# Optimization experiments

Measured on AMD Instinct MI355X. Metric: run time of the kernel, lower is better.

Reference implementation:

```python
import jax, jax.numpy as jnp
import numpy as np

M, K, N = 4096, 4096, 11008

def setup_inputs() -> dict:
    key = jax.random.key(0)
    k1, k2, k3, k4 = jax.random.split(key, 4)
    x = jax.random.normal(k1, (M, K), dtype=jnp.float32)
    weight = jax.random.randint(k2, (K, N), 0, 127, dtype=jnp.int32)
    antiquant_scale = jax.random.uniform(k3, (N,), dtype=jnp.float32)
    antiquant_offset = jax.random.normal(k4, (N,), dtype=jnp.float32)
    return {"x": x, "weight": weight, "antiquant_scale": antiquant_scale, "antiquant_offset": antiquant_offset}

def reference(x, weight, antiquant_scale, antiquant_offset):
    # Dequantize: (w + offset) * scale, per output channel (broadcast over K)
    dequantized_weight = (weight.astype(jnp.float32) + antiquant_offset) * antiquant_scale  # [K, N]
    return jnp.matmul(x, dequantized_weight)  # [M, N]
```

## Files before the change

### kernel.cpp

```cpp
#include <hip/hip_runtime.h>
#include <hip/hip_bf16.h>
#include <stdint.h>

#define M_DIM 4096
#define K_DIM 4096
#define N_DIM 11008
#define BKT 64
#define NT (K_DIM / BKT)
#define GRID_MN 688
#define NBLK_M 16

typedef __attribute__((ext_vector_type(8))) short short8;
typedef __attribute__((ext_vector_type(4))) float floatx4;

__device__ __forceinline__ short f2bf(float f) {
  union { float f; uint32_t u; } c; c.f = f;
  uint32_t u = c.u;
  u += 0x7FFFu + ((u >> 16) & 1u);
  return (short)(u >> 16);
}

__device__ __forceinline__ void gload_lds16(const void* g, void* l) {
  __builtin_amdgcn_global_load_lds(
      (const __attribute__((address_space(1))) unsigned int*)g,
      (__attribute__((address_space(3))) unsigned int*)l, 16, 0, 0);
}

__global__ __launch_bounds__(256) void convert_x_kernel(const float* __restrict__ x,
                                                        short* __restrict__ xb,
                                                        float* __restrict__ rowsum) {
  const int m = blockIdx.x;
  const int t = threadIdx.x;
  const float* row = x + (size_t)m * K_DIM + t * 16;
  short* orow = xb + (size_t)m * K_DIM + t * 16;
  float4 v0 = *(const float4*)(row + 0);
  float4 v1 = *(const float4*)(row + 4);
  float4 v2 = *(const float4*)(row + 8);
  float4 v3 = *(const float4*)(row + 12);
  float sum = v0.x + v0.y + v0.z + v0.w
            + v1.x + v1.y + v1.z + v1.w
            + v2.x + v2.y + v2.z + v2.w
            + v3.x + v3.y + v3.z + v3.w;
  short8 o0, o1;
  o0[0] = f2bf(v0.x); o0[1] = f2bf(v0.y); o0[2] = f2bf(v0.z); o0[3] = f2bf(v0.w);
  o0[4] = f2bf(v1.x); o0[5] = f2bf(v1.y); o0[6] = f2bf(v1.z); o0[7] = f2bf(v1.w);
  o1[0] = f2bf(v2.x); o1[1] = f2bf(v2.y); o1[2] = f2bf(v2.z); o1[3] = f2bf(v2.w);
  o1[4] = f2bf(v3.x); o1[5] = f2bf(v3.y); o1[6] = f2bf(v3.z); o1[7] = f2bf(v3.w);
  *(short8*)(orow) = o0;
  *(short8*)(orow + 8) = o1;
  #pragma unroll
  for (int off = 32; off > 0; off >>= 1) sum += __shfl_down(sum, off);
  __shared__ float part[4];
  if ((t & 63) == 0) part[t >> 6] = sum;
  __syncthreads();
  if (t == 0) rowsum[m] = part[0] + part[1] + part[2] + part[3];
}

__global__ __launch_bounds__(256) void convert_w_kernel(const int* __restrict__ w,
                                                        short* __restrict__ wt) {
  __shared__ short tile[64][72];
  const int bk = blockIdx.x * 64;
  const int bn = blockIdx.y * 64;
  const int t = threadIdx.x;
  const int kr = t >> 2;
  const int c0 = (t & 3) * 16;
  const int* src = w + (size_t)(bk + kr) * N_DIM + bn + c0;
  int4 a = *(const int4*)(src + 0);
  int4 b = *(const int4*)(src + 4);
  int4 c = *(const int4*)(src + 8);
  int4 d = *(const int4*)(src + 12);
  short* dst = &tile[kr][c0];
  dst[0]  = f2bf((float)a.x); dst[1]  = f2bf((float)a.y);
  dst[2]  = f2bf((float)a.z); dst[3]  = f2bf((float)a.w);
  dst[4]  = f2bf((float)b.x); dst[5]  = f2bf((float)b.y);
  dst[6]  = f2bf((float)b.z); dst[7]  = f2bf((float)b.w);
  dst[8]  = f2bf((float)c.x); dst[9]  = f2bf((float)c.y);
  dst[10] = f2bf((float)c.z); dst[11] = f2bf((float)c.w);
  dst[12] = f2bf((float)d.x); dst[13] = f2bf((float)d.y);
  dst[14] = f2bf((float)d.z); dst[15] = f2bf((float)d.w);
  __syncthreads();
  const int nr = t >> 2;
  short8 o0, o1;
  #pragma unroll
  for (int j = 0; j < 8; ++j) o0[j] = tile[c0 + j][nr];
  #pragma unroll
  for (int j = 0; j < 8; ++j) o1[j] = tile[c0 + 8 + j][nr];
  short* odst = wt + (size_t)(bn + nr) * K_DIM + bk + c0;
  *(short8*)(odst) = o0;
  *(short8*)(odst + 8) = o1;
}

__global__ __launch_bounds__(512, 2) void gemm_kernel(const short* __restrict__ xb,
                                                      const short* __restrict__ wt,
                                                      const float* __restrict__ scale,
                                                      const float* __restrict__ offset,
                                                      const float* __restrict__ rowsum,
                                                      float* __restrict__ out) {
  __shared__ short lds[2][4][8192];
  const int tid = threadIdx.x;
  const int bid = blockIdx.x;
  const int wg = (bid & 7) * (GRID_MN / 8) + (bid >> 3);
  const int bm = (wg % NBLK_M) * 256;
  const int bn = (wg / NBLK_M) * 256;

  const int wid = tid >> 6;
  const int lane = tid & 63;
  const int wr = wid >> 2;
  const int wc = wid & 3;
  const int hb = wc >> 1;
  const int lr = lane & 15;
  const int lg = lane >> 4;
  const int swz = lr & 7;
  const int gk0 = (lg ^ swz) * 8;
  const int gk1 = ((lg ^ 4) ^ swz) * 8;
  const int brow = (wc & 1) * 64 + lr;

  const int srow = tid >> 3;
  const int glog = (tid & 7) ^ (srow & 7);

  auto stage = [&](const short* opbase, int rowbase, int half, int kt, short* region) {
    const short* s0 = opbase + (size_t)(rowbase + half * 128 + srow) * K_DIM + kt * BKT + glog * 8;
    gload_lds16(s0, (char*)region + tid * 16);
    const short* s1 = opbase + (size_t)(rowbase + half * 128 + srow + 64) * K_DIM + kt * BKT + glog * 8;
    gload_lds16(s1, (char*)region + (tid + 512) * 16);
  };

  floatx4 acc[8][4];
  const floatx4 zero = {0.f, 0.f, 0.f, 0.f};
  #pragma unroll
  for (int i = 0; i < 8; ++i)
    #pragma unroll
    for (int j = 0; j < 4; ++j) acc[i][j] = zero;

  stage(xb, bm, 0, 0, &lds[0][0][0]);
  stage(xb, bm, 1, 0, &lds[0][1][0]);
  stage(wt, bn, 0, 0, &lds[0][2][0]);
  stage(wt, bn, 1, 0, &lds[0][3][0]);
  stage(wt, bn, 0, 1, &lds[1][2][0]);
  stage(xb, bm, 0, 1, &lds[1][0][0]);
  stage(wt, bn, 1, 1, &lds[1][3][0]);
  asm volatile("s_waitcnt vmcnt(6)" ::: "memory");
  __builtin_amdgcn_s_barrier();

  short8 a03[4][2], a47[4][2], b0[2][2], b1[2][2];
  {
    const short* As = &lds[0][wr][0];
    #pragma unroll
    for (int mf = 0; mf < 4; ++mf) {
      const short* p = As + (mf * 16 + lr) * 64;
      a03[mf][0] = *(const short8*)(p + gk0);
      a03[mf][1] = *(const short8*)(p + gk1);
    }
  }

  for (int s = 0; s < NT; ++s) {
    const int beta = s & 1;
    const short* As = &lds[beta][wr][0];
    const short* Bs = &lds[beta][2 + hb][0];

    #pragma unroll
    for (int nf = 0; nf < 2; ++nf) {
      const short* p = Bs + (brow + nf * 16) * 64;
      b0[nf][0] = *(const short8*)(p + gk0);
      b0[nf][1] = *(const short8*)(p + gk1);
      const short* q = Bs + (brow + (nf + 2) * 16) * 64;
      b1[nf][0] = *(const short8*)(q + gk0);
      b1[nf][1] = *(const short8*)(q + gk1);
    }
    asm volatile("s_waitcnt lgkmcnt(8)" ::: "memory");
    if (s + 1 < NT) stage(xb, bm, 1, s + 1, &lds[beta ^ 1][1][0]);
    __builtin_amdgcn_s_barrier();
    asm volatile("s_waitcnt lgkmcnt(0)" ::: "memory");
    __builtin_amdgcn_s_setprio(1);
    #pragma unroll
    for (int mf = 0; mf < 4; ++mf)
      #pragma unroll
      for (int nf = 0; nf < 2; ++nf) {
        acc[mf][nf] = __builtin_amdgcn_mfma_f32_16x16x32_bf16(a03[mf][0], b0[nf][0], acc[mf][nf], 0, 0, 0);
        acc[mf][nf] = __builtin_amdgcn_mfma_f32_16x16x32_bf16(a03[mf][1], b0[nf][1], acc[mf][nf], 0, 0, 0);
      }
    __builtin_amdgcn_s_setprio(0);
    __builtin_amdgcn_s_barrier();

    #pragma unroll
    for (int mf = 0; mf < 4; ++mf) {
      const short* p = As + ((mf + 4) * 16 + lr) * 64;
      a47[mf][0] = *(const short8*)(p + gk0);
      a47[mf][1] = *(const short8*)(p + gk1);
    }
    if (s + 2 < NT) stage(wt, bn, 0, s + 2, &lds[beta][2][0]);
    __builtin_amdgcn_s_barrier();
    asm volatile("s_waitcnt lgkmcnt(0)" ::: "memory");
    __builtin_amdgcn_s_setprio(1);
    #pragma unroll
    for (int mf = 0; mf < 4; ++mf)
      #pragma unroll
      for (int nf = 0; nf < 2; ++nf) {
        acc[mf + 4][nf] = __builtin_amdgcn_mfma_f32_16x16x32_bf16(a47[mf][0], b0[nf][0], acc[mf + 4][nf], 0, 0, 0);
        acc[mf + 4][nf] = __builtin_amdgcn_mfma_f32_16x16x32_bf16(a47[mf][1], b0[nf][1], acc[mf + 4][nf], 0, 0, 0);
      }
    __builtin_amdgcn_s_setprio(0);
    __builtin_amdgcn_s_barrier();

    if (s + 2 < NT) stage(xb, bm, 0, s + 2, &lds[beta][0][0]);
    __builtin_amdgcn_s_barrier();
    __builtin_amdgcn_s_setprio(1);
    #pragma unroll
    for (int mf = 0; mf < 4; ++mf)
      #pragma unroll
      for (int nf = 0; nf < 2; ++nf) {
        acc[mf][nf + 2] = __builtin_amdgcn_mfma_f32_16x16x32_bf16(a03[mf][0], b1[nf][0], acc[mf][nf + 2], 0, 0, 0);
        acc[mf][nf + 2] = __builtin_amdgcn_mfma_f32_16x16x32_bf16(a03[mf][1], b1[nf][1], acc[mf][nf + 2], 0, 0, 0);
      }
    __builtin_amdgcn_s_setprio(0);
    __builtin_amdgcn_s_barrier();

    if (s + 2 < NT) {
      stage(wt, bn, 1, s + 2, &lds[beta][3][0]);
      asm volatile("s_waitcnt vmcnt(6)" ::: "memory");
    } else {
      asm volatile("s_waitcnt vmcnt(0)" ::: "memory");
    }
    __builtin_amdgcn_s_barrier();
    if (s + 1 < NT) {
      const short* An = &lds[beta ^ 1][wr][0];
      #pragma unroll
      for (int mf = 0; mf < 4; ++mf) {
        const short* p = An + (mf * 16 + lr) * 64;
        a03[mf][0] = *(const short8*)(p + gk0);
        a03[mf][1] = *(const short8*)(p + gk1);
      }
    }
    __builtin_amdgcn_s_setprio(1);
    #pragma unroll
    for (int mf = 0; mf < 4; ++mf)
      #pragma unroll
      for (int nf = 0; nf < 2; ++nf) {
        acc[mf + 4][nf + 2] = __builtin_amdgcn_mfma_f32_16x16x32_bf16(a47[mf][0], b1[nf][0], acc[mf + 4][nf + 2], 0, 0, 0);
        acc[mf + 4][nf + 2] = __builtin_amdgcn_mfma_f32_16x16x32_bf16(a47[mf][1], b1[nf][1], acc[mf + 4][nf + 2], 0, 0, 0);
      }
    __builtin_amdgcn_s_setprio(0);
    __builtin_amdgcn_s_barrier();
  }

  const int orow0 = bm + wr * 128 + lg * 4;
  const int ocol0 = bn + wc * 64 + lr;
  float4 rsv[8];
  #pragma unroll
  for (int amf = 0; amf < 8; ++amf)
    rsv[amf] = *(const float4*)&rowsum[orow0 + amf * 16];
  #pragma unroll
  for (int anf = 0; anf < 4; ++anf) {
    const int n = ocol0 + anf * 16;
    const float sc = scale[n];
    const float of = offset[n];
    #pragma unroll
    for (int amf = 0; amf < 8; ++amf) {
      const int mbase = orow0 + amf * 16;
      const float4 rv = rsv[amf];
      out[(size_t)(mbase + 0) * N_DIM + n] = (acc[amf][anf][0] + of * rv.x) * sc;
      out[(size_t)(mbase + 1) * N_DIM + n] = (acc[amf][anf][1] + of * rv.y) * sc;
      out[(size_t)(mbase + 2) * N_DIM + n] = (acc[amf][anf][2] + of * rv.z) * sc;
      out[(size_t)(mbase + 3) * N_DIM + n] = (acc[amf][anf][3] + of * rv.w) * sc;
    }
  }
}

__global__ __launch_bounds__(256) void fallback_gemm(const float* __restrict__ x,
                                                     const int* __restrict__ w,
                                                     const float* __restrict__ scale,
                                                     const float* __restrict__ offset,
                                                     float* __restrict__ out) {
  __shared__ float xs[32][33];
  __shared__ float bs[32][33];
  const int bm = blockIdx.y * 32, bn = blockIdx.x * 32;
  const int t = threadIdx.x;
  const int tm = t >> 5, tn = t & 31;
  float acc[4] = {0.f, 0.f, 0.f, 0.f};
  for (int k0 = 0; k0 < K_DIM; k0 += 32) {
    #pragma unroll
    for (int i = 0; i < 4; ++i) {
      int idx = t + i * 256; int r = idx >> 5, c = idx & 31;
      xs[r][c] = x[(size_t)(bm + r) * K_DIM + k0 + c];
      bs[r][c] = ((float)w[(size_t)(k0 + r) * N_DIM + bn + c] + offset[bn + c]) * scale[bn + c];
    }
    __syncthreads();
    #pragma unroll 8
    for (int kk = 0; kk < 32; ++kk) {
      float wv = bs[kk][tn];
      #pragma unroll
      for (int i = 0; i < 4; ++i) acc[i] += xs[tm + 8 * i][kk] * wv;
    }
    __syncthreads();
  }
  #pragma unroll
  for (int i = 0; i < 4; ++i)
    out[(size_t)(bm + tm + 8 * i) * N_DIM + bn + tn] = acc[i];
}

extern "C" void kernel_launch(void* const* d_in, const int* in_sizes, int n_in,
                              void* d_out, int out_size, void* d_ws, size_t ws_size,
                              hipStream_t stream) {
  const float* x      = (const float*)d_in[0];
  const int*   w      = (const int*)d_in[1];
  const float* scale  = (const float*)d_in[2];
  const float* offset = (const float*)d_in[3];
  float* out = (float*)d_out;

  const size_t xb_bytes = (size_t)M_DIM * K_DIM * 2;
  const size_t wt_bytes = (size_t)N_DIM * K_DIM * 2;
  const size_t rs_bytes = (size_t)M_DIM * 4;

  if (ws_size >= xb_bytes + wt_bytes + rs_bytes) {
    short* xb = (short*)d_ws;
    short* wt = (short*)((char*)d_ws + xb_bytes);
    float* rowsum = (float*)((char*)d_ws + xb_bytes + wt_bytes);
    convert_x_kernel<<<M_DIM, 256, 0, stream>>>(x, xb, rowsum);
    convert_w_kernel<<<dim3(K_DIM / 64, N_DIM / 64), 256, 0, stream>>>(w, wt);
    gemm_kernel<<<GRID_MN, 512, 0, stream>>>(xb, wt, scale, offset, rowsum, out);
  } else {
    fallback_gemm<<<dim3(N_DIM / 32, M_DIM / 32), 256, 0, stream>>>(x, w, scale, offset, out);
  }
}
```

Measured before the change: 423.6 us.

## Restructure main loop schedule to overlap LDS fragment loads with MFMA phases

Reorders the software pipeline of the bf16 MFMA main loop. b0 fragments for the next tile are now loaded alongside a03 at the end of each iteration, and b1 and a47 reads are interleaved between MFMA quadrants with partial lgkmcnt waits. Global-to-LDS staging is redistributed across the phases, and the prologue prefetch order changes to wait for the first tile fully. The intent is fewer barriers per iteration (five instead of eight) and LDS reads hidden behind MFMA work. The risk is more live registers and subtle LDS race hazards from the new wait counts.

```diff
diff --git a/kernel.cpp b/kernel.cpp
--- a/kernel.cpp
+++ b/kernel.cpp
@@ -136,10 +136,7 @@
   stage(xb, bm, 1, 0, &lds[0][1][0]);
   stage(wt, bn, 0, 0, &lds[0][2][0]);
   stage(wt, bn, 1, 0, &lds[0][3][0]);
-  stage(wt, bn, 0, 1, &lds[1][2][0]);
-  stage(xb, bm, 0, 1, &lds[1][0][0]);
-  stage(wt, bn, 1, 1, &lds[1][3][0]);
-  asm volatile("s_waitcnt vmcnt(6)" ::: "memory");
+  asm volatile("s_waitcnt vmcnt(0)" ::: "memory");
   __builtin_amdgcn_s_barrier();
 
   short8 a03[4][2], a47[4][2], b0[2][2], b1[2][2];
@@ -151,36 +148,22 @@
       a03[mf][0] = *(const short8*)(p + gk0);
       a03[mf][1] = *(const short8*)(p + gk1);
     }
-  }
-
-  for (int s = 0; s < NT; ++s) {
-    const int beta = s & 1;
-    const short* As = &lds[beta][wr][0];
-    const short* Bs = &lds[beta][2 + hb][0];
-
+    const short* Bsp = &lds[0][2 + hb][0];
     #pragma unroll
     for (int nf = 0; nf < 2; ++nf) {
-      const short* p = Bs + (brow + nf * 16) * 64;
+      const short* p = Bsp + (brow + nf * 16) * 64;
       b0[nf][0] = *(const short8*)(p + gk0);
       b0[nf][1] = *(const short8*)(p + gk1);
-      const short* q = Bs + (brow + (nf + 2) * 16) * 64;
-      b1[nf][0] = *(const short8*)(q + gk0);
-      b1[nf][1] = *(const short8*)(q + gk1);
-    }
-    asm volatile("s_waitcnt lgkmcnt(8)" ::: "memory");
-    if (s + 1 < NT) stage(xb, bm, 1, s + 1, &lds[beta ^ 1][1][0]);
-    __builtin_amdgcn_s_barrier();
-    asm volatile("s_waitcnt lgkmcnt(0)" ::: "memory");
-    __builtin_amdgcn_s_setprio(1);
-    #pragma unroll
-    for (int mf = 0; mf < 4; ++mf)
-      #pragma unroll
-      for (int nf = 0; nf < 2; ++nf) {
-        acc[mf][nf] = __builtin_amdgcn_mfma_f32_16x16x32_bf16(a03[mf][0], b0[nf][0], acc[mf][nf], 0, 0, 0);
-        acc[mf][nf] = __builtin_amdgcn_mfma_f32_16x16x32_bf16(a03[mf][1], b0[nf][1], acc[mf][nf], 0, 0, 0);
-      }
-    __builtin_amdgcn_s_setprio(0);
-    __builtin_amdgcn_s_barrier();
+    }
+  }
+  stage(xb, bm, 0, 1, &lds[1][0][0]);
+  stage(wt, bn, 0, 1, &lds[1][2][0]);
+  stage(wt, bn, 1, 1, &lds[1][3][0]);
+
+  for (int u = 0; u < NT; ++u) {
+    const int g = u & 1;
+    const short* As = &lds[g][wr][0];
+    const short* Bs = &lds[g][2 + hb][0];
 
     #pragma unroll
     for (int mf = 0; mf < 4; ++mf) {
@@ -188,9 +171,28 @@
       a47[mf][0] = *(const short8*)(p + gk0);
       a47[mf][1] = *(const short8*)(p + gk1);
     }
-    if (s + 2 < NT) stage(wt, bn, 0, s + 2, &lds[beta][2][0]);
+    asm volatile("s_waitcnt lgkmcnt(8)" ::: "memory");
     __builtin_amdgcn_s_barrier();
-    asm volatile("s_waitcnt lgkmcnt(0)" ::: "memory");
+    if (u + 1 < NT) stage(xb, bm, 1, u + 1, &lds[g ^ 1][1][0]);
+    __builtin_amdgcn_s_setprio(1);
+    #pragma unroll
+    for (int mf = 0; mf < 4; ++mf)
+      #pragma unroll
+      for (int nf = 0; nf < 2; ++nf) {
+        acc[mf][nf] = __builtin_amdgcn_mfma_f32_16x16x32_bf16(a03[mf][0], b0[nf][0], acc[mf][nf], 0, 0, 0);
+        acc[mf][nf] = __builtin_amdgcn_mfma_f32_16x16x32_bf16(a03[mf][1], b0[nf][1], acc[mf][nf], 0, 0, 0);
+      }
+    __builtin_amdgcn_s_setprio(0);
+
+    #pragma unroll
+    for (int nf = 0; nf < 2; ++nf) {
+      const short* q = Bs + (brow + (nf + 2) * 16) * 64;
+      b1[nf][0] = *(const short8*)(q + gk0);
+      b1[nf][1] = *(const short8*)(q + gk1);
+    }
+    asm volatile("s_waitcnt lgkmcnt(4)" ::: "memory");
+    __builtin_amdgcn_s_barrier();
+    if (u + 2 < NT) stage(xb, bm, 0, u + 2, &lds[g][0][0]);
     __builtin_amdgcn_s_setprio(1);
     #pragma unroll
     for (int mf = 0; mf < 4; ++mf)
@@ -200,10 +202,10 @@
         acc[mf + 4][nf] = __builtin_amdgcn_mfma_f32_16x16x32_bf16(a47[mf][1], b0[nf][1], acc[mf + 4][nf], 0, 0, 0);
       }
     __builtin_amdgcn_s_setprio(0);
+
+    asm volatile("s_waitcnt lgkmcnt(0)" ::: "memory");
     __builtin_amdgcn_s_barrier();
-
-    if (s + 2 < NT) stage(xb, bm, 0, s + 2, &lds[beta][0][0]);
-    __builtin_amdgcn_s_barrier();
+    if (u + 2 < NT) stage(wt, bn, 0, u + 2, &lds[g][2][0]);
     __builtin_amdgcn_s_setprio(1);
     #pragma unroll
     for (int mf = 0; mf < 4; ++mf)
@@ -213,23 +215,29 @@
         acc[mf][nf + 2] = __builtin_amdgcn_mfma_f32_16x16x32_bf16(a03[mf][1], b1[nf][1], acc[mf][nf + 2], 0, 0, 0);
       }
     __builtin_amdgcn_s_setprio(0);
-    __builtin_amdgcn_s_barrier();
-
-    if (s + 2 < NT) {
-      stage(wt, bn, 1, s + 2, &lds[beta][3][0]);
+
+    if (u + 2 < NT) {
+      stage(wt, bn, 1, u + 2, &lds[g][3][0]);
       asm volatile("s_waitcnt vmcnt(6)" ::: "memory");
     } else {
       asm volatile("s_waitcnt vmcnt(0)" ::: "memory");
     }
     __builtin_amdgcn_s_barrier();
-    if (s + 1 < NT) {
-      const short* An = &lds[beta ^ 1][wr][0];
+    if (u + 1 < NT) {
+      const short* An = &lds[g ^ 1][wr][0];
+      const short* Bn = &lds[g ^ 1][2 + hb][0];
       #pragma unroll
       for (int mf = 0; mf < 4; ++mf) {
         const short* p = An + (mf * 16 + lr) * 64;
         a03[mf][0] = *(const short8*)(p + gk0);
         a03[mf][1] = *(const short8*)(p + gk1);
       }
+      #pragma unroll
+      for (int nf = 0; nf < 2; ++nf) {
+        const short* p = Bn + (brow + nf * 16) * 64;
+        b0[nf][0] = *(const short8*)(p + gk0);
+        b0[nf][1] = *(const short8*)(p + gk1);
+      }
     }
     __builtin_amdgcn_s_setprio(1);
     #pragma unroll
@@ -240,7 +248,6 @@
         acc[mf + 4][nf + 2] = __builtin_amdgcn_mfma_f32_16x16x32_bf16(a47[mf][1], b1[nf][1], acc[mf + 4][nf + 2], 0, 0, 0);
       }
     __builtin_amdgcn_s_setprio(0);
-    __builtin_amdgcn_s_barrier();
   }
 
   const int orow0 = bm + wr * 128 + lg * 4;
```

Result: faster. 405.0 us, median of 2 (-4.4%).

## Restructure GEMM main loop: unroll by two, reschedule LDS reads and barriers

Applied to the files above, without the earlier changes.

Unrolls the K loop by two so the double-buffer index is a compile-time constant, and replaces per-call address recomputation with incrementing global pointers. It also moves the fragment loads: a47 and b1 are read earlier and the next tile's b0 is prefetched together with a03. The number of barriers per step drops from eight to four. The aim is to cut address arithmetic and synchronisation overhead and overlap LDS reads with MFMA, at the risk of LDS read/write hazards with the new wait counts.

```diff
diff --git a/kernel.cpp b/kernel.cpp
--- a/kernel.cpp
+++ b/kernel.cpp
@@ -118,11 +118,15 @@
   const int srow = tid >> 3;
   const int glog = (tid & 7) ^ (srow & 7);
 
-  auto stage = [&](const short* opbase, int rowbase, int half, int kt, short* region) {
-    const short* s0 = opbase + (size_t)(rowbase + half * 128 + srow) * K_DIM + kt * BKT + glog * 8;
-    gload_lds16(s0, (char*)region + tid * 16);
-    const short* s1 = opbase + (size_t)(rowbase + half * 128 + srow + 64) * K_DIM + kt * BKT + glog * 8;
-    gload_lds16(s1, (char*)region + (tid + 512) * 16);
+  const size_t toff = (size_t)srow * K_DIM + glog * 8;
+  const short* pA0 = xb + (size_t)bm * K_DIM + toff;
+  const short* pA1 = xb + ((size_t)bm + 128) * K_DIM + toff;
+  const short* pB0 = wt + (size_t)bn * K_DIM + toff;
+  const short* pB1 = wt + ((size_t)bn + 128) * K_DIM + toff;
+
+  auto stage2 = [&](const short* p, short* region) {
+    gload_lds16(p, (char*)region + tid * 16);
+    gload_lds16(p + (size_t)64 * K_DIM, (char*)region + (tid + 512) * 16);
   };
 
   floatx4 acc[8][4];
@@ -132,116 +136,142 @@
     #pragma unroll
     for (int j = 0; j < 4; ++j) acc[i][j] = zero;
 
-  stage(xb, bm, 0, 0, &lds[0][0][0]);
-  stage(xb, bm, 1, 0, &lds[0][1][0]);
-  stage(wt, bn, 0, 0, &lds[0][2][0]);
-  stage(wt, bn, 1, 0, &lds[0][3][0]);
-  stage(wt, bn, 0, 1, &lds[1][2][0]);
-  stage(xb, bm, 0, 1, &lds[1][0][0]);
-  stage(wt, bn, 1, 1, &lds[1][3][0]);
+  stage2(pA0, &lds[0][0][0]);
+  stage2(pA1, &lds[0][1][0]);
+  stage2(pB0, &lds[0][2][0]);
+  stage2(pB1, &lds[0][3][0]);
+  stage2(pB0 + BKT, &lds[1][2][0]);
+  stage2(pA0 + BKT, &lds[1][0][0]);
+  stage2(pB1 + BKT, &lds[1][3][0]);
   asm volatile("s_waitcnt vmcnt(6)" ::: "memory");
   __builtin_amdgcn_s_barrier();
+  pA1 += BKT;
+  pA0 += 2 * BKT;
+  pB0 += 2 * BKT;
+  pB1 += 2 * BKT;
+
+  const short* const AsB[2] = {&lds[0][wr][0], &lds[1][wr][0]};
+  const short* const BsB[2] = {&lds[0][2 + hb][0], &lds[1][2 + hb][0]};
 
   short8 a03[4][2], a47[4][2], b0[2][2], b1[2][2];
   {
-    const short* As = &lds[0][wr][0];
+    const short* As = AsB[0];
     #pragma unroll
     for (int mf = 0; mf < 4; ++mf) {
       const short* p = As + (mf * 16 + lr) * 64;
       a03[mf][0] = *(const short8*)(p + gk0);
       a03[mf][1] = *(const short8*)(p + gk1);
     }
-  }
-
-  for (int s = 0; s < NT; ++s) {
-    const int beta = s & 1;
-    const short* As = &lds[beta][wr][0];
-    const short* Bs = &lds[beta][2 + hb][0];
-
+    const short* Bsp = BsB[0];
     #pragma unroll
     for (int nf = 0; nf < 2; ++nf) {
-      const short* p = Bs + (brow + nf * 16) * 64;
+      const short* p = Bsp + (brow + nf * 16) * 64;
       b0[nf][0] = *(const short8*)(p + gk0);
       b0[nf][1] = *(const short8*)(p + gk1);
-      const short* q = Bs + (brow + (nf + 2) * 16) * 64;
-      b1[nf][0] = *(const short8*)(q + gk0);
-      b1[nf][1] = *(const short8*)(q + gk1);
-    }
-    asm volatile("s_waitcnt lgkmcnt(8)" ::: "memory");
-    if (s + 1 < NT) stage(xb, bm, 1, s + 1, &lds[beta ^ 1][1][0]);
-    __builtin_amdgcn_s_barrier();
-    asm volatile("s_waitcnt lgkmcnt(0)" ::: "memory");
-    __builtin_amdgcn_s_setprio(1);
-    #pragma unroll
-    for (int mf = 0; mf < 4; ++mf)
-      #pragma unroll
-      for (int nf = 0; nf < 2; ++nf) {
-        acc[mf][nf] = __builtin_amdgcn_mfma_f32_16x16x32_bf16(a03[mf][0], b0[nf][0], acc[mf][nf], 0, 0, 0);
-        acc[mf][nf] = __builtin_amdgcn_mfma_f32_16x16x32_bf16(a03[mf][1], b0[nf][1], acc[mf][nf], 0, 0, 0);
-      }
-    __builtin_amdgcn_s_setprio(0);
-    __builtin_amdgcn_s_barrier();
-
-    #pragma unroll
-    for (int mf = 0; mf < 4; ++mf) {
-      const short* p = As + ((mf + 4) * 16 + lr) * 64;
-      a47[mf][0] = *(const short8*)(p + gk0);
-      a47[mf][1] = *(const short8*)(p + gk1);
-    }
-    if (s + 2 < NT) stage(wt, bn, 0, s + 2, &lds[beta][2][0]);
-    __builtin_amdgcn_s_barrier();
-    asm volatile("s_waitcnt lgkmcnt(0)" ::: "memory");
-    __builtin_amdgcn_s_setprio(1);
-    #pragma unroll
-    for (int mf = 0; mf < 4; ++mf)
-      #pragma unroll
-      for (int nf = 0; nf < 2; ++nf) {
-        acc[mf + 4][nf] = __builtin_amdgcn_mfma_f32_16x16x32_bf16(a47[mf][0], b0[nf][0], acc[mf + 4][nf], 0, 0, 0);
-        acc[mf + 4][nf] = __builtin_amdgcn_mfma_f32_16x16x32_bf16(a47[mf][1], b0[nf][1], acc[mf + 4][nf], 0, 0, 0);
-      }
-    __builtin_amdgcn_s_setprio(0);
-    __builtin_amdgcn_s_barrier();
-
-    if (s + 2 < NT) stage(xb, bm, 0, s + 2, &lds[beta][0][0]);
-    __builtin_amdgcn_s_barrier();
-    __builtin_amdgcn_s_setprio(1);
-    #pragma unroll
-    for (int mf = 0; mf < 4; ++mf)
-      #pragma unroll
-      for (int nf = 0; nf < 2; ++nf) {
-        acc[mf][nf + 2] = __builtin_amdgcn_mfma_f32_16x16x32_bf16(a03[mf][0], b1[nf][0], acc[mf][nf + 2], 0, 0, 0);
-        acc[mf][nf + 2] = __builtin_amdgcn_mfma_f32_16x16x32_bf16(a03[mf][1], b1[nf][1], acc[mf][nf + 2], 0, 0, 0);
-      }
-    __builtin_amdgcn_s_setprio(0);
-    __builtin_amdgcn_s_barrier();
-
-    if (s + 2 < NT) {
-      stage(wt, bn, 1, s + 2, &lds[beta][3][0]);
-      asm volatile("s_waitcnt vmcnt(6)" ::: "memory");
-    } else {
-      asm volatile("s_waitcnt vmcnt(0)" ::: "memory");
-    }
-    __builtin_amdgcn_s_barrier();
-    if (s + 1 < NT) {
-      const short* An = &lds[beta ^ 1][wr][0];
-      #pragma unroll
-      for (int mf = 0; mf < 4; ++mf) {
-        const short* p = An + (mf * 16 + lr) * 64;
-        a03[mf][0] = *(const short8*)(p + gk0);
-        a03[mf][1] = *(const short8*)(p + gk1);
-      }
-    }
-    __builtin_amdgcn_s_setprio(1);
-    #pragma unroll
-    for (int mf = 0; mf < 4; ++mf)
-      #pragma unroll
-      for (int nf = 0; nf < 2; ++nf) {
-        acc[mf + 4][nf + 2] = __builtin_amdgcn_mfma_f32_16x16x32_bf16(a47[mf][0], b1[nf][0], acc[mf + 4][nf + 2], 0, 0, 0);
-        acc[mf + 4][nf + 2] = __builtin_amdgcn_mfma_f32_16x16x32_bf16(a47[mf][1], b1[nf][1], acc[mf + 4][nf + 2], 0, 0, 0);
-      }
-    __builtin_amdgcn_s_setprio(0);
-    __builtin_amdgcn_s_barrier();
-  }
+    }
+  }
+
+#define STEP_BODY(G, GN)                                                       \
+  {                                                                            \
+    const short* As = AsB[G];                                                  \
+    const short* Bs = BsB[G];                                                  \
+                    \
+    _Pragma("unroll")                                                          \
+    for (int mf = 0; mf < 4; ++mf) {                                           \
+      const short* p = As + ((mf + 4) * 16 + lr) * 64;                         \
+      a47[mf][0] = *(const short8*)(p + gk0);                                  \
+      a47[mf][1] = *(const short8*)(p + gk1);                                  \
+    }                                                                          \
+    asm volatile("s_waitcnt lgkmcnt(8)" ::: "memory");                         \
+    __builtin_amdgcn_s_barrier();                                              \
+    if (u + 1 < NT) stage2(pA1, &lds[GN][1][0]);                               \
+    pA1 += BKT;                                                                \
+    __builtin_amdgcn_s_setprio(1);                                             \
+    _Pragma("unroll")                                                          \
+    for (int mf = 0; mf < 4; ++mf)                                             \
+      _Pragma("unroll")                                                        \
+      for (int nf = 0; nf < 2; ++nf) {                                         \
+        acc[mf][nf] = __builtin_amdgcn_mfma_f32_16x16x32_bf16(a03[mf][0], b0[nf][0], acc[mf][nf], 0, 0, 0); \
+        acc[mf][nf] = __builtin_amdgcn_mfma_f32_16x16x32_bf16(a03[mf][1], b0[nf][1], acc[mf][nf], 0, 0, 0); \
+      }                                                                        \
+    __builtin_amdgcn_s_setprio(0);                                             \
+                      \
+    _Pragma("unroll")                                                          \
+    for (int nf = 0; nf < 2; ++nf) {                                           \
+      const short* q = Bs + (brow + (nf + 2) * 16) * 64;                       \
+      b1[nf][0] = *(const short8*)(q + gk0);                                   \
+      b1[nf][1] = *(const short8*)(q + gk1);                                   \
+    }                                                                          \
+    asm volatile("s_waitcnt lgkmcnt(4)" ::: "memory");                         \
+    __builtin_amdgcn_s_barrier();                                              \
+    if (u + 2 < NT) stage2(pA0, &lds[G][0][0]);                                \
+    pA0 += BKT;                                                                \
+    __builtin_amdgcn_s_setprio(1);                                             \
+    _Pragma("unroll")                                                          \
+    for (int mf = 0; mf < 4; ++mf)                                             \
+      _Pragma("unroll")                                                        \
+      for (int nf = 0; nf < 2; ++nf) {                                         \
+        acc[mf + 4][nf] = __builtin_amdgcn_mfma_f32_16x16x32_bf16(a47[mf][0], b0[nf][0], acc[mf + 4][nf], 0, 0, 0); \
+        acc[mf + 4][nf] = __builtin_amdgcn_mfma_f32_16x16x32_bf16(a47[mf][1], b0[nf][1], acc[mf + 4][nf], 0, 0, 0); \
+      }                                                                        \
+    __builtin_amdgcn_s_setprio(0);                                             \
+                                  \
+    asm volatile("s_waitcnt lgkmcnt(0)" ::: "memory");                         \
+    __builtin_amdgcn_s_barrier();                                              \
+    if (u + 2 < NT) stage2(pB0, &lds[G][2][0]);                                \
+    pB0 += BKT;                                                                \
+    __builtin_amdgcn_s_setprio(1);                                             \
+    _Pragma("unroll")                                                          \
+    for (int mf = 0; mf < 4; ++mf)                                             \
+      _Pragma("unroll")                                                        \
+      for (int nf = 0; nf < 2; ++nf) {                                         \
+        acc[mf][nf + 2] = __builtin_amdgcn_mfma_f32_16x16x32_bf16(a03[mf][0], b1[nf][0], acc[mf][nf + 2], 0, 0, 0); \
+        acc[mf][nf + 2] = __builtin_amdgcn_mfma_f32_16x16x32_bf16(a03[mf][1], b1[nf][1], acc[mf][nf + 2], 0, 0, 0); \
+      }                                                                        \
+    __builtin_amdgcn_s_setprio(0);                                             \
+      \
+    if (u + 2 < NT) {                                                          \
+      stage2(pB1, &lds[G][3][0]);                                              \
+      asm volatile("s_waitcnt vmcnt(6)" ::: "memory");                         \
+    } else {                                                                   \
+      asm volatile("s_waitcnt vmcnt(0)" ::: "memory");                         \
+    }                                                                          \
+    pB1 += BKT;                                                                \
+    __builtin_amdgcn_s_barrier();                                              \
+    if (u + 1 < NT) {                                                          \
+      const short* An = AsB[GN];                                               \
+      const short* Bn = BsB[GN];                                               \
+      _Pragma("unroll")                                                        \
+      for (int mf = 0; mf < 4; ++mf) {                                         \
+        const short* p = An + (mf * 16 + lr) * 64;                             \
+        a03[mf][0] = *(const short8*)(p + gk0);                                \
+        a03[mf][1] = *(const short8*)(p + gk1);                                \
+      }                                                                        \
+      _Pragma("unroll")                                                        \
+      for (int nf = 0; nf < 2; ++nf) {                                         \
+        const short* p = Bn + (brow + nf * 16) * 64;                           \
+        b0[nf][0] = *(const short8*)(p + gk0);                                 \
+        b0[nf][1] = *(const short8*)(p + gk1);                                 \
+      }                                                                        \
+    }                                                                          \
+    __builtin_amdgcn_s_setprio(1);                                             \
+    _Pragma("unroll")                                                          \
+    for (int mf = 0; mf < 4; ++mf)                                             \
+      _Pragma("unroll")                                                        \
+      for (int nf = 0; nf < 2; ++nf) {                                         \
+        acc[mf + 4][nf + 2] = __builtin_amdgcn_mfma_f32_16x16x32_bf16(a47[mf][0], b1[nf][0], acc[mf + 4][nf + 2], 0, 0, 0); \
+        acc[mf + 4][nf + 2] = __builtin_amdgcn_mfma_f32_16x16x32_bf16(a47[mf][1], b1[nf][1], acc[mf + 4][nf + 2], 0, 0, 0); \
+      }                                                                        \
+    __builtin_amdgcn_s_setprio(0);                                             \
+  }
+
+  for (int u = 0; u < NT; u += 2) {
+    STEP_BODY(0, 1)
+    ++u;
+    STEP_BODY(1, 0)
+    --u;
+  }
+#undef STEP_BODY
 
   const int orow0 = bm + wr * 128 + lg * 4;
   const int ocol0 = bn + wc * 64 + lr;
```

Result: faster. 405.6 us (-4.2%).

## Unroll K-loop by two with incremental pointers and reordered LDS staging schedule

Applied to the files above, without the earlier changes.

Restructures the main GEMM loop into a two-stage unrolled form with compile-time buffer indices. Global-to-LDS source pointers are precomputed and advanced incrementally, which removes per-stage address arithmetic. The staging order and the B-fragment reads are changed, with B1 now read just before its quadrant, and the vmcnt waits are adjusted. Sched barriers after the lgkm waits are added and the tail is peeled. This aims to cut scalar/VALU overhead and improve overlap, but it adds code size and needs the wait counts to match the new issue order.

```diff
diff --git a/kernel.cpp b/kernel.cpp
--- a/kernel.cpp
+++ b/kernel.cpp
@@ -12,6 +12,13 @@
 
 typedef __attribute__((ext_vector_type(8))) short short8;
 typedef __attribute__((ext_vector_type(4))) float floatx4;
+
+#define MFMA16 __builtin_amdgcn_mfma_f32_16x16x32_bf16
+#define BAR() __builtin_amdgcn_s_barrier()
+#define LGKM0() do { asm volatile("s_waitcnt lgkmcnt(0)" ::: "memory"); __builtin_amdgcn_sched_barrier(0); } while (0)
+#define LGKM8() asm volatile("s_waitcnt lgkmcnt(8)" ::: "memory")
+#define VM4() asm volatile("s_waitcnt vmcnt(4)" ::: "memory")
+#define VM0() asm volatile("s_waitcnt vmcnt(0)" ::: "memory")
 
 __device__ __forceinline__ short f2bf(float f) {
   union { float f; uint32_t u; } c; c.f = f;
@@ -117,12 +124,15 @@
 
   const int srow = tid >> 3;
   const int glog = (tid & 7) ^ (srow & 7);
-
-  auto stage = [&](const short* opbase, int rowbase, int half, int kt, short* region) {
-    const short* s0 = opbase + (size_t)(rowbase + half * 128 + srow) * K_DIM + kt * BKT + glog * 8;
-    gload_lds16(s0, (char*)region + tid * 16);
-    const short* s1 = opbase + (size_t)(rowbase + half * 128 + srow + 64) * K_DIM + kt * BKT + glog * 8;
-    gload_lds16(s1, (char*)region + (tid + 512) * 16);
+  const size_t toff = (size_t)srow * K_DIM + glog * 8;
+  const short* pAh0 = xb + (size_t)bm * K_DIM + toff;
+  const short* pAh1 = xb + ((size_t)bm + 128) * K_DIM + toff;
+  const short* pBh0 = wt + (size_t)bn * K_DIM + toff;
+  const short* pBh1 = wt + ((size_t)bn + 128) * K_DIM + toff;
+
+  auto stage2 = [&](const short* p, short* region) {
+    gload_lds16(p, (char*)region + tid * 16);
+    gload_lds16(p + (size_t)64 * K_DIM, (char*)region + (tid + 512) * 16);
   };
 
   floatx4 acc[8][4];
@@ -132,116 +142,144 @@
     #pragma unroll
     for (int j = 0; j < 4; ++j) acc[i][j] = zero;
 
-  stage(xb, bm, 0, 0, &lds[0][0][0]);
-  stage(xb, bm, 1, 0, &lds[0][1][0]);
-  stage(wt, bn, 0, 0, &lds[0][2][0]);
-  stage(wt, bn, 1, 0, &lds[0][3][0]);
-  stage(wt, bn, 0, 1, &lds[1][2][0]);
-  stage(xb, bm, 0, 1, &lds[1][0][0]);
-  stage(wt, bn, 1, 1, &lds[1][3][0]);
-  asm volatile("s_waitcnt vmcnt(6)" ::: "memory");
-  __builtin_amdgcn_s_barrier();
-
   short8 a03[4][2], a47[4][2], b0[2][2], b1[2][2];
-  {
-    const short* As = &lds[0][wr][0];
+  const short* const As[2] = {&lds[0][wr][0], &lds[1][wr][0]};
+  const short* const Bs[2] = {&lds[0][2 + hb][0], &lds[1][2 + hb][0]};
+
+  auto rdA03 = [&](const short* A) {
     #pragma unroll
     for (int mf = 0; mf < 4; ++mf) {
-      const short* p = As + (mf * 16 + lr) * 64;
+      const short* p = A + (mf * 16 + lr) * 64;
       a03[mf][0] = *(const short8*)(p + gk0);
       a03[mf][1] = *(const short8*)(p + gk1);
     }
-  }
-
-  for (int s = 0; s < NT; ++s) {
-    const int beta = s & 1;
-    const short* As = &lds[beta][wr][0];
-    const short* Bs = &lds[beta][2 + hb][0];
-
+  };
+  auto rdA47 = [&](const short* A) {
+    #pragma unroll
+    for (int mf = 0; mf < 4; ++mf) {
+      const short* p = A + ((mf + 4) * 16 + lr) * 64;
+      a47[mf][0] = *(const short8*)(p + gk0);
+      a47[mf][1] = *(const short8*)(p + gk1);
+    }
+  };
+  auto rdB0 = [&](const short* B) {
     #pragma unroll
     for (int nf = 0; nf < 2; ++nf) {
-      const short* p = Bs + (brow + nf * 16) * 64;
+      const short* p = B + (brow + nf * 16) * 64;
       b0[nf][0] = *(const short8*)(p + gk0);
       b0[nf][1] = *(const short8*)(p + gk1);
-      const short* q = Bs + (brow + (nf + 2) * 16) * 64;
-      b1[nf][0] = *(const short8*)(q + gk0);
-      b1[nf][1] = *(const short8*)(q + gk1);
-    }
-    asm volatile("s_waitcnt lgkmcnt(8)" ::: "memory");
-    if (s + 1 < NT) stage(xb, bm, 1, s + 1, &lds[beta ^ 1][1][0]);
-    __builtin_amdgcn_s_barrier();
-    asm volatile("s_waitcnt lgkmcnt(0)" ::: "memory");
+    }
+  };
+  auto rdB1 = [&](const short* B) {
+    #pragma unroll
+    for (int nf = 0; nf < 2; ++nf) {
+      const short* p = B + (brow + (nf + 2) * 16) * 64;
+      b1[nf][0] = *(const short8*)(p + gk0);
+      b1[nf][1] = *(const short8*)(p + gk1);
+    }
+  };
+  auto q00 = [&]() {
     __builtin_amdgcn_s_setprio(1);
     #pragma unroll
     for (int mf = 0; mf < 4; ++mf)
       #pragma unroll
       for (int nf = 0; nf < 2; ++nf) {
-        acc[mf][nf] = __builtin_amdgcn_mfma_f32_16x16x32_bf16(a03[mf][0], b0[nf][0], acc[mf][nf], 0, 0, 0);
-        acc[mf][nf] = __builtin_amdgcn_mfma_f32_16x16x32_bf16(a03[mf][1], b0[nf][1], acc[mf][nf], 0, 0, 0);
+        acc[mf][nf] = MFMA16(a03[mf][0], b0[nf][0], acc[mf][nf], 0, 0, 0);
+        acc[mf][nf] = MFMA16(a03[mf][1], b0[nf][1], acc[mf][nf], 0, 0, 0);
       }
     __builtin_amdgcn_s_setprio(0);
-    __builtin_amdgcn_s_barrier();
-
-    #pragma unroll
-    for (int mf = 0; mf < 4; ++mf) {
-      const short* p = As + ((mf + 4) * 16 + lr) * 64;
-      a47[mf][0] = *(const short8*)(p + gk0);
-      a47[mf][1] = *(const short8*)(p + gk1);
-    }
-    if (s + 2 < NT) stage(wt, bn, 0, s + 2, &lds[beta][2][0]);
-    __builtin_amdgcn_s_barrier();
-    asm volatile("s_waitcnt lgkmcnt(0)" ::: "memory");
+  };
+  auto q10 = [&]() {
     __builtin_amdgcn_s_setprio(1);
     #pragma unroll
     for (int mf = 0; mf < 4; ++mf)
       #pragma unroll
       for (int nf = 0; nf < 2; ++nf) {
-        acc[mf + 4][nf] = __builtin_amdgcn_mfma_f32_16x16x32_bf16(a47[mf][0], b0[nf][0], acc[mf + 4][nf], 0, 0, 0);
-        acc[mf + 4][nf] = __builtin_amdgcn_mfma_f32_16x16x32_bf16(a47[mf][1], b0[nf][1], acc[mf + 4][nf], 0, 0, 0);
+        acc[mf + 4][nf] = MFMA16(a47[mf][0], b0[nf][0], acc[mf + 4][nf], 0, 0, 0);
+        acc[mf + 4][nf] = MFMA16(a47[mf][1], b0[nf][1], acc[mf + 4][nf], 0, 0, 0);
       }
     __builtin_amdgcn_s_setprio(0);
-    __builtin_amdgcn_s_barrier();
-
-    if (s + 2 < NT) stage(xb, bm, 0, s + 2, &lds[beta][0][0]);
-    __builtin_amdgcn_s_barrier();
+  };
+  auto q01 = [&]() {
     __builtin_amdgcn_s_setprio(1);
     #pragma unroll
     for (int mf = 0; mf < 4; ++mf)
       #pragma unroll
       for (int nf = 0; nf < 2; ++nf) {
-        acc[mf][nf + 2] = __builtin_amdgcn_mfma_f32_16x16x32_bf16(a03[mf][0], b1[nf][0], acc[mf][nf + 2], 0, 0, 0);
-        acc[mf][nf + 2] = __builtin_amdgcn_mfma_f32_16x16x32_bf16(a03[mf][1], b1[nf][1], acc[mf][nf + 2], 0, 0, 0);
+        acc[mf][nf + 2] = MFMA16(a03[mf][0], b1[nf][0], acc[mf][nf + 2], 0, 0, 0);
+        acc[mf][nf + 2] = MFMA16(a03[mf][1], b1[nf][1], acc[mf][nf + 2], 0, 0, 0);
       }
     __builtin_amdgcn_s_setprio(0);
-    __builtin_amdgcn_s_barrier();
-
-    if (s + 2 < NT) {
-      stage(wt, bn, 1, s + 2, &lds[beta][3][0]);
-      asm volatile("s_waitcnt vmcnt(6)" ::: "memory");
-    } else {
-      asm volatile("s_waitcnt vmcnt(0)" ::: "memory");
-    }
-    __builtin_amdgcn_s_barrier();
-    if (s + 1 < NT) {
-      const short* An = &lds[beta ^ 1][wr][0];
-      #pragma unroll
-      for (int mf = 0; mf < 4; ++mf) {
-        const short* p = An + (mf * 16 + lr) * 64;
-        a03[mf][0] = *(const short8*)(p + gk0);
-        a03[mf][1] = *(const short8*)(p + gk1);
-      }
-    }
+  };
+  auto q11 = [&]() {
     __builtin_amdgcn_s_setprio(1);
     #pragma unroll
     for (int mf = 0; mf < 4; ++mf)
       #pragma unroll
       for (int nf = 0; nf < 2; ++nf) {
-        acc[mf + 4][nf + 2] = __builtin_amdgcn_mfma_f32_16x16x32_bf16(a47[mf][0], b1[nf][0], acc[mf + 4][nf + 2], 0, 0, 0);
-        acc[mf + 4][nf + 2] = __builtin_amdgcn_mfma_f32_16x16x32_bf16(a47[mf][1], b1[nf][1], acc[mf + 4][nf + 2], 0, 0, 0);
+        acc[mf + 4][nf + 2] = MFMA16(a47[mf][0], b1[nf][0], acc[mf + 4][nf + 2], 0, 0, 0);
+        acc[mf + 4][nf + 2] = MFMA16(a47[mf][1], b1[nf][1], acc[mf + 4][nf + 2], 0, 0, 0);
       }
     __builtin_amdgcn_s_setprio(0);
-    __builtin_amdgcn_s_barrier();
+  };
+
+  stage2(pAh0, &lds[0][0][0]); pAh0 += BKT;
+  stage2(pBh0, &lds[0][2][0]); pBh0 += BKT;
+  stage2(pAh1, &lds[0][1][0]); pAh1 += BKT;
+  stage2(pBh1, &lds[0][3][0]); pBh1 += BKT;
+  stage2(pAh0, &lds[1][0][0]); pAh0 += BKT;
+  stage2(pBh0, &lds[1][2][0]); pBh0 += BKT;
+  VM4();
+  BAR();
+
+  for (int i = 0; i < NT / 2 - 1; ++i) {
+    rdA03(As[0]); rdB0(Bs[0]);
+    stage2(pAh1, &lds[1][1][0]); pAh1 += BKT;
+    LGKM8();
+    BAR(); LGKM0(); q00(); BAR();
+    rdA47(As[0]);
+    stage2(pBh1, &lds[1][3][0]); pBh1 += BKT;
+    BAR(); LGKM0(); q10(); BAR();
+    rdB1(Bs[0]);
+    stage2(pAh0, &lds[0][0][0]); pAh0 += BKT;
+    BAR(); LGKM0(); q01(); BAR();
+    stage2(pBh0, &lds[0][2][0]); pBh0 += BKT;
+    VM4();
+    BAR(); q11(); BAR();
+    rdA03(As[1]); rdB0(Bs[1]);
+    stage2(pAh1, &lds[0][1][0]); pAh1 += BKT;
+    LGKM8();
+    BAR(); LGKM0(); q00(); BAR();
+    rdA47(As[1]);
+    stage2(pBh1, &lds[0][3][0]); pBh1 += BKT;
+    BAR(); LGKM0(); q10(); BAR();
+    rdB1(Bs[1]);
+    stage2(pAh0, &lds[1][0][0]); pAh0 += BKT;
+    BAR(); LGKM0(); q01(); BAR();
+    stage2(pBh0, &lds[1][2][0]); pBh0 += BKT;
+    VM4();
+    BAR(); q11(); BAR();
   }
+
+  rdA03(As[0]); rdB0(Bs[0]);
+  stage2(pAh1, &lds[1][1][0]);
+  LGKM8();
+  BAR(); LGKM0(); q00(); BAR();
+  rdA47(As[0]);
+  stage2(pBh1, &lds[1][3][0]);
+  BAR(); LGKM0(); q10(); BAR();
+  rdB1(Bs[0]);
+  BAR(); LGKM0(); q01(); BAR();
+  VM0();
+  BAR(); q11(); BAR();
+  rdA03(As[1]); rdB0(Bs[1]);
+  LGKM8();
+  BAR(); LGKM0(); q00(); BAR();
+  rdA47(As[1]);
+  BAR(); LGKM0(); q10(); BAR();
+  rdB1(Bs[1]);
+  BAR(); LGKM0(); q01(); BAR();
+  q11();
 
   const int orow0 = bm + wr * 128 + lg * 4;
   const int ocol0 = bn + wc * 64 + lr;
```

After: 428.7 us. Within noise of the previous version (+1.2%).
